# Performance work log

Hardware: AMD Instinct MI355X
Metric: run time of the kernel (lower is better)

Reference implementation:

```python
import jax, jax.numpy as jnp
import numpy as np

DT = 0.1  # Euler timestep (init kwarg)

def setup_inputs() -> dict:
    key = jax.random.key(0)
    ks = jax.random.split(key, 6)
    B, L, S, U, H = 1024, 512, 64, 32, 512
    return {
        "initial_state": jax.random.normal(ks[0], (B, S), dtype=jnp.float32),
        "control_inputs": jax.random.normal(ks[1], (B, L, U), dtype=jnp.float32),
        "W1": jax.random.normal(ks[2], (S + U, H), dtype=jnp.float32) * (1.0 / np.sqrt(S + U)),
        "b1": jnp.zeros((H,), dtype=jnp.float32),
        "W2": jax.random.normal(ks[3], (H, S), dtype=jnp.float32) * (1.0 / np.sqrt(H)),
        "b2": jnp.zeros((S,), dtype=jnp.float32),
    }

def reference(initial_state, control_inputs, W1, b1, W2, b2):
    # Euler integration: state_{t+1} = state_t + dt * f(state_t, u_t)
    # f is a 2-layer tanh MLP on the concatenated [state, control].
    def step(state, u):
        z = jnp.concatenate([state, u], axis=-1)        # (B, S+U)
        diff = jnp.tanh(z @ W1 + b1) @ W2 + b2          # (B, S)
        new_state = state + diff * DT
        return new_state, new_state

    u_seq = jnp.swapaxes(control_inputs, 0, 1)          # (L, B, U)
    _, states = jax.lax.scan(step, initial_state, u_seq)  # (L, B, S)
    return jnp.swapaxes(states, 0, 1)                   # (B, L, S)
```

## Files before the change

kernel.cpp:

```cpp
#include <hip/hip_runtime.h>
#include <hip/hip_fp16.h>


typedef _Float16 f16;
typedef __attribute__((ext_vector_type(4))) _Float16 f16x4;
typedef __attribute__((ext_vector_type(8))) _Float16 f16x8;
typedef __attribute__((ext_vector_type(4))) float f32x4;

#define MFMA16(a, b, c) __builtin_amdgcn_mfma_f32_16x16x32_f16((a), (b), (c), 0, 0, 0)

__device__ __forceinline__ float tanh_fast(float x) {
    float t = __builtin_amdgcn_exp2f(x * 2.885390081777927f);
    float r = __builtin_amdgcn_rcpf(t + 1.0f);
    return __builtin_fmaf(-2.0f, r, 1.0f);
}

__global__ __launch_bounds__(512, 2)
void euler_kernel(const float* __restrict__ init,
                  const float* __restrict__ uin,
                  const float* __restrict__ W1,
                  const float* __restrict__ b1,
                  const float* __restrict__ W2,
                  const float* __restrict__ b2,
                  float* __restrict__ out) {
    const int L = 512, S = 64, U = 32, H = 512;
    const int tid  = threadIdx.x;
    const int lane = tid & 63;
    const int w    = tid >> 6;
    const int g    = lane >> 4;
    const int r16  = lane & 15;
    const int b0   = blockIdx.x * 16;

    __shared__ f16   zbuf[6 * 64 * 8];
    __shared__ float pbuf[8 * 16 * 16 * 4];

    f16x8 W1F[6][4];
    #pragma unroll
    for (int kk = 0; kk < 6; ++kk)
      #pragma unroll
      for (int nf = 0; nf < 4; ++nf) {
          const int hcol = w * 64 + 32 * (nf >> 1) + 8 * (r16 >> 2) + 4 * (nf & 1) + (r16 & 3);
          #pragma unroll
          for (int j = 0; j < 8; ++j) {
              int k  = kk * 32 + g * 8 + j;
              int kr = (k < 128) ? (k & 63) : (64 + (k & 31));
              W1F[kk][nf][j] = (f16)W1[kr * H + hcol];
          }
      }
    f32x4 b1v[4];
    #pragma unroll
    for (int nf = 0; nf < 4; ++nf)
        b1v[nf] = *(const f32x4*)&b1[w * 64 + 32 * (nf >> 1) + 4 * (nf & 1) + 8 * g];

    f16x8 W2F[2][4];
    #pragma unroll
    for (int a = 0; a < 2; ++a)
      #pragma unroll
      for (int nf2 = 0; nf2 < 4; ++nf2)
        #pragma unroll
        for (int j = 0; j < 8; ++j) {
            int k = w * 64 + a * 32 + g * 8 + j;
            W2F[a][nf2][j] = (f16)W2[k * S + nf2 * 16 + r16];
        }

    f32x4 b2v = (f32x4){0.f, 0.f, 0.f, 0.f};
    f32x4 stateF = (f32x4){0.f, 0.f, 0.f, 0.f};
    f32x4 ua0 = (f32x4){0.f, 0.f, 0.f, 0.f}, ua1 = ua0;
    const int schunk = (w >> 1) * 64 + ((w & 1) * 2 + (g >> 1)) * 16 + r16;
    const int soff   = (g & 1) * 4;

    if (w < 4) {
        b2v    = *(const f32x4*)&b2[w * 16 + g * 4];
        stateF = *(const f32x4*)&init[(size_t)(b0 + r16) * S + w * 16 + g * 4];
        f16x4 sh, sl;
        #pragma unroll
        for (int j = 0; j < 4; ++j) {
            sh[j] = (f16)stateF[j];
            sl[j] = (f16)(stateF[j] - (float)sh[j]);
        }
        *(f16x4*)&zbuf[schunk * 8 + soff]         = sh;
        *(f16x4*)&zbuf[(schunk + 128) * 8 + soff] = sl;
    } else if (w == 4 || w == 5) {
        const float* up = uin + (size_t)(b0 + r16) * L * U + g * 8;
        f32x4 u0 = *(const f32x4*)up;
        f32x4 u1 = *(const f32x4*)(up + 4);
        f16x8 uv;
        if (w == 4) {
            #pragma unroll
            for (int j = 0; j < 4; ++j) { uv[j] = (f16)u0[j]; uv[4 + j] = (f16)u1[j]; }
            *(f16x8*)&zbuf[(256 + lane) * 8] = uv;
        } else {
            #pragma unroll
            for (int j = 0; j < 4; ++j) {
                uv[j]     = (f16)(u0[j] - (float)(f16)u0[j]);
                uv[4 + j] = (f16)(u1[j] - (float)(f16)u1[j]);
            }
            *(f16x8*)&zbuf[(320 + lane) * 8] = uv;
        }
        ua0 = *(const f32x4*)(up + U);
        ua1 = *(const f32x4*)(up + U + 4);
    }
    __syncthreads();

    #pragma unroll 1
    for (int t = 0; t < L; ++t) {
        f16x8 zf[6];
        #pragma unroll
        for (int kk = 0; kk < 6; ++kk)
            zf[kk] = *(const f16x8*)&zbuf[(kk * 64 + lane) * 8];
        f32x4 acc1[4];
        #pragma unroll
        for (int nf = 0; nf < 4; ++nf) acc1[nf] = b1v[nf];
        #pragma unroll
        for (int kk = 0; kk < 6; ++kk)
          #pragma unroll
          for (int nf = 0; nf < 4; ++nf)
            acc1[nf] = MFMA16(W1F[kk][nf], zf[kk], acc1[nf]);
        f16x8 hb[2];
        #pragma unroll
        for (int a = 0; a < 2; ++a)
          #pragma unroll
          for (int j8 = 0; j8 < 8; ++j8)
            hb[a][j8] = (f16)tanh_fast(acc1[a * 2 + (j8 >> 2)][j8 & 3]);
        f32x4 acc2[4];
        #pragma unroll
        for (int nf2 = 0; nf2 < 4; ++nf2) acc2[nf2] = (f32x4){0.f, 0.f, 0.f, 0.f};
        #pragma unroll
        for (int a = 0; a < 2; ++a)
          #pragma unroll
          for (int nf2 = 0; nf2 < 4; ++nf2)
            acc2[nf2] = MFMA16(W2F[a][nf2], hb[a], acc2[nf2]);
        #pragma unroll
        for (int nf2 = 0; nf2 < 4; ++nf2)
            *(f32x4*)&pbuf[(w * 256 + nf2 * 64 + lane) * 4] = acc2[nf2];
        __syncthreads();

        if (w < 4) {
            f32x4 sum = *(const f32x4*)&pbuf[(w * 64 + lane) * 4];
            #pragma unroll
            for (int ww = 1; ww < 8; ++ww) {
                f32x4 p = *(const f32x4*)&pbuf[(ww * 256 + w * 64 + lane) * 4];
                #pragma unroll
                for (int j = 0; j < 4; ++j) sum[j] += p[j];
            }
            f16x4 sh, sl;
            #pragma unroll
            for (int j = 0; j < 4; ++j) {
                float d = sum[j] + b2v[j];
                float s = __builtin_fmaf(0.1f, d, stateF[j]);
                stateF[j] = s;
                sh[j] = (f16)s;
                sl[j] = (f16)(s - (float)sh[j]);
            }
            *(f32x4*)&out[((size_t)(b0 + r16) * L + t) * S + w * 16 + g * 4] = stateF;
            *(f16x4*)&zbuf[schunk * 8 + soff]         = sh;
            *(f16x4*)&zbuf[(schunk + 128) * 8 + soff] = sl;
        } else if (w == 4 || w == 5) {
            if (t + 1 < L) {
                f16x8 uv;
                if (w == 4) {
                    #pragma unroll
                    for (int j = 0; j < 4; ++j) { uv[j] = (f16)ua0[j]; uv[4 + j] = (f16)ua1[j]; }
                    *(f16x8*)&zbuf[(256 + lane) * 8] = uv;
                } else {
                    #pragma unroll
                    for (int j = 0; j < 4; ++j) {
                        uv[j]     = (f16)(ua0[j] - (float)(f16)ua0[j]);
                        uv[4 + j] = (f16)(ua1[j] - (float)(f16)ua1[j]);
                    }
                    *(f16x8*)&zbuf[(320 + lane) * 8] = uv;
                }
            }
            if (t + 2 < L) {
                const float* up = uin + (size_t)(b0 + r16) * L * U + (size_t)(t + 2) * U + g * 8;
                ua0 = *(const f32x4*)up;
                ua1 = *(const f32x4*)(up + 4);
            }
        }
        __syncthreads();
    }
}

extern "C" void kernel_launch(void* const* d_in, const int* in_sizes, int n_in,
                              void* d_out, int out_size, void* d_ws, size_t ws_size,
                              hipStream_t stream) {
    const float* init = (const float*)d_in[0];
    const float* uin  = (const float*)d_in[1];
    const float* W1   = (const float*)d_in[2];
    const float* b1   = (const float*)d_in[3];
    const float* W2   = (const float*)d_in[4];
    const float* b2   = (const float*)d_in[5];
    euler_kernel<<<dim3(64), dim3(512), 0, stream>>>(init, uin, W1, b1, W2, b2,
                                                     (float*)d_out);
}
```

Before: 600.6 us.

## Precompute control-input layer-1 contribution off critical path; spread reduction across all waves

Each wave now computes the control-input part of the first-layer MFMA (hi/lo split) for the next step in registers during the current step, so the per-step dependent chain only runs four K-chunks on the state instead of six. The cross-wave reduction of layer-2 partials and the state update are spread over all eight waves (two outputs per lane) instead of four. The __syncthreads calls are replaced by a raw s_barrier preceded by an LDS-only waitcnt. This cuts serial latency per timestep but adds redundant u-MFMAs in every wave and more barrier-sensitive LDS traffic.

```diff
diff --git a/kernel.cpp b/kernel.cpp
--- a/kernel.cpp
+++ b/kernel.cpp
@@ -3,11 +3,16 @@
 
 
 typedef _Float16 f16;
-typedef __attribute__((ext_vector_type(4))) _Float16 f16x4;
+typedef __attribute__((ext_vector_type(2))) _Float16 f16x2;
 typedef __attribute__((ext_vector_type(8))) _Float16 f16x8;
+typedef __attribute__((ext_vector_type(2))) float f32x2;
 typedef __attribute__((ext_vector_type(4))) float f32x4;
 
 #define MFMA16(a, b, c) __builtin_amdgcn_mfma_f32_16x16x32_f16((a), (b), (c), 0, 0, 0)
+
+#define BAR() do { asm volatile("s_waitcnt lgkmcnt(0)" ::: "memory"); \
+                   __builtin_amdgcn_s_barrier();                      \
+                   asm volatile("" ::: "memory"); } while (0)
 
 __device__ __forceinline__ float tanh_fast(float x) {
     float t = __builtin_amdgcn_exp2f(x * 2.885390081777927f);
@@ -31,10 +36,11 @@
     const int r16  = lane & 15;
     const int b0   = blockIdx.x * 16;
 
-    __shared__ f16   zbuf[6 * 64 * 8];
-    __shared__ float pbuf[8 * 16 * 16 * 4];
+    __shared__ f16   zbuf[256 * 8];
+    __shared__ float pbuf[8 * 256 * 4];
 
-    f16x8 W1F[6][4];
+    f16x8 W1F[4][4];
+    f16x8 W1Fu[2][4];
     #pragma unroll
     for (int kk = 0; kk < 6; ++kk)
       #pragma unroll
@@ -44,7 +50,8 @@
           for (int j = 0; j < 8; ++j) {
               int k  = kk * 32 + g * 8 + j;
               int kr = (k < 128) ? (k & 63) : (64 + (k & 31));
-              W1F[kk][nf][j] = (f16)W1[kr * H + hcol];
+              f16 v  = (f16)W1[kr * H + hcol];
+              if (kk < 4) W1F[kk][nf][j] = v; else W1Fu[kk - 4][nf][j] = v;
           }
       }
     f32x4 b1v[4];
@@ -63,56 +70,53 @@
             W2F[a][nf2][j] = (f16)W2[k * S + nf2 * 16 + r16];
         }
 
-    f32x4 b2v = (f32x4){0.f, 0.f, 0.f, 0.f};
-    f32x4 stateF = (f32x4){0.f, 0.f, 0.f, 0.f};
-    f32x4 ua0 = (f32x4){0.f, 0.f, 0.f, 0.f}, ua1 = ua0;
-    const int schunk = (w >> 1) * 64 + ((w & 1) * 2 + (g >> 1)) * 16 + r16;
-    const int soff   = (g & 1) * 4;
+    f32x2 b2v    = *(const f32x2*)&b2[w * 8 + g * 2];
+    f32x2 stateF = *(const f32x2*)&init[(size_t)(b0 + r16) * S + w * 8 + g * 2];
+    const int zci = ((w >> 2) * 64 + (w & 3) * 16 + r16) * 8 + g * 2;
+    {
+        f16 h0 = (f16)stateF[0], h1 = (f16)stateF[1];
+        f16x2 hi2, lo2;
+        hi2[0] = h0;                              hi2[1] = h1;
+        lo2[0] = (f16)(stateF[0] - (float)h0);    lo2[1] = (f16)(stateF[1] - (float)h1);
+        *(f16x2*)&zbuf[zci]        = hi2;
+        *(f16x2*)&zbuf[zci + 1024] = lo2;
+    }
 
-    if (w < 4) {
-        b2v    = *(const f32x4*)&b2[w * 16 + g * 4];
-        stateF = *(const f32x4*)&init[(size_t)(b0 + r16) * S + w * 16 + g * 4];
-        f16x4 sh, sl;
+    const float* uptr = uin + (size_t)(b0 + r16) * L * U + g * 8;
+    f32x4 ua0 = *(const f32x4*)uptr;
+    f32x4 ua1 = *(const f32x4*)(uptr + 4);
+    f32x4 uacc[4];
+    #pragma unroll
+    for (int nf = 0; nf < 4; ++nf) uacc[nf] = b1v[nf];
+    {
+        f16x8 uh, ul;
         #pragma unroll
         for (int j = 0; j < 4; ++j) {
-            sh[j] = (f16)stateF[j];
-            sl[j] = (f16)(stateF[j] - (float)sh[j]);
+            f16 h0 = (f16)ua0[j]; uh[j] = h0;     ul[j] = (f16)(ua0[j] - (float)h0);
+            f16 h1 = (f16)ua1[j]; uh[4 + j] = h1; ul[4 + j] = (f16)(ua1[j] - (float)h1);
         }
-        *(f16x4*)&zbuf[schunk * 8 + soff]         = sh;
-        *(f16x4*)&zbuf[(schunk + 128) * 8 + soff] = sl;
-    } else if (w == 4 || w == 5) {
-        const float* up = uin + (size_t)(b0 + r16) * L * U + g * 8;
-        f32x4 u0 = *(const f32x4*)up;
-        f32x4 u1 = *(const f32x4*)(up + 4);
-        f16x8 uv;
-        if (w == 4) {
-            #pragma unroll
-            for (int j = 0; j < 4; ++j) { uv[j] = (f16)u0[j]; uv[4 + j] = (f16)u1[j]; }
-            *(f16x8*)&zbuf[(256 + lane) * 8] = uv;
-        } else {
-            #pragma unroll
-            for (int j = 0; j < 4; ++j) {
-                uv[j]     = (f16)(u0[j] - (float)(f16)u0[j]);
-                uv[4 + j] = (f16)(u1[j] - (float)(f16)u1[j]);
-            }
-            *(f16x8*)&zbuf[(320 + lane) * 8] = uv;
-        }
-        ua0 = *(const f32x4*)(up + U);
-        ua1 = *(const f32x4*)(up + U + 4);
+        #pragma unroll
+        for (int nf = 0; nf < 4; ++nf) uacc[nf] = MFMA16(W1Fu[0][nf], uh, uacc[nf]);
+        #pragma unroll
+        for (int nf = 0; nf < 4; ++nf) uacc[nf] = MFMA16(W1Fu[1][nf], ul, uacc[nf]);
     }
-    __syncthreads();
+    ua0 = *(const f32x4*)(uptr + U);
+    ua1 = *(const f32x4*)(uptr + U + 4);
+    BAR();
+
+    const int pbase = ((w >> 1) * 64 + (2 * (w & 1) + (g >> 1)) * 16 + r16) * 4 + 2 * (g & 1);
 
     #pragma unroll 1
     for (int t = 0; t < L; ++t) {
-        f16x8 zf[6];
+        f16x8 zf[4];
         #pragma unroll
-        for (int kk = 0; kk < 6; ++kk)
+        for (int kk = 0; kk < 4; ++kk)
             zf[kk] = *(const f16x8*)&zbuf[(kk * 64 + lane) * 8];
         f32x4 acc1[4];
         #pragma unroll
-        for (int nf = 0; nf < 4; ++nf) acc1[nf] = b1v[nf];
+        for (int nf = 0; nf < 4; ++nf) acc1[nf] = uacc[nf];
         #pragma unroll
-        for (int kk = 0; kk < 6; ++kk)
+        for (int kk = 0; kk < 4; ++kk)
           #pragma unroll
           for (int nf = 0; nf < 4; ++nf)
             acc1[nf] = MFMA16(W1F[kk][nf], zf[kk], acc1[nf]);
@@ -133,51 +137,47 @@
         #pragma unroll
         for (int nf2 = 0; nf2 < 4; ++nf2)
             *(f32x4*)&pbuf[(w * 256 + nf2 * 64 + lane) * 4] = acc2[nf2];
-        __syncthreads();
 
-        if (w < 4) {
-            f32x4 sum = *(const f32x4*)&pbuf[(w * 64 + lane) * 4];
-            #pragma unroll
-            for (int ww = 1; ww < 8; ++ww) {
-                f32x4 p = *(const f32x4*)&pbuf[(ww * 256 + w * 64 + lane) * 4];
-                #pragma unroll
-                for (int j = 0; j < 4; ++j) sum[j] += p[j];
-            }
-            f16x4 sh, sl;
+        #pragma unroll
+        for (int nf = 0; nf < 4; ++nf) uacc[nf] = b1v[nf];
+        {
+            f16x8 uh, ul;
             #pragma unroll
             for (int j = 0; j < 4; ++j) {
-                float d = sum[j] + b2v[j];
-                float s = __builtin_fmaf(0.1f, d, stateF[j]);
-                stateF[j] = s;
-                sh[j] = (f16)s;
-                sl[j] = (f16)(s - (float)sh[j]);
+                f16 h0 = (f16)ua0[j]; uh[j] = h0;     ul[j] = (f16)(ua0[j] - (float)h0);
+                f16 h1 = (f16)ua1[j]; uh[4 + j] = h1; ul[4 + j] = (f16)(ua1[j] - (float)h1);
             }
-            *(f32x4*)&out[((size_t)(b0 + r16) * L + t) * S + w * 16 + g * 4] = stateF;
-            *(f16x4*)&zbuf[schunk * 8 + soff]         = sh;
-            *(f16x4*)&zbuf[(schunk + 128) * 8 + soff] = sl;
-        } else if (w == 4 || w == 5) {
-            if (t + 1 < L) {
-                f16x8 uv;
-                if (w == 4) {
-                    #pragma unroll
-                    for (int j = 0; j < 4; ++j) { uv[j] = (f16)ua0[j]; uv[4 + j] = (f16)ua1[j]; }
-                    *(f16x8*)&zbuf[(256 + lane) * 8] = uv;
-                } else {
-                    #pragma unroll
-                    for (int j = 0; j < 4; ++j) {
-                        uv[j]     = (f16)(ua0[j] - (float)(f16)ua0[j]);
-                        uv[4 + j] = (f16)(ua1[j] - (float)(f16)ua1[j]);
-                    }
-                    *(f16x8*)&zbuf[(320 + lane) * 8] = uv;
-                }
-            }
-            if (t + 2 < L) {
-                const float* up = uin + (size_t)(b0 + r16) * L * U + (size_t)(t + 2) * U + g * 8;
-                ua0 = *(const f32x4*)up;
-                ua1 = *(const f32x4*)(up + 4);
-            }
+            #pragma unroll
+            for (int nf = 0; nf < 4; ++nf) uacc[nf] = MFMA16(W1Fu[0][nf], uh, uacc[nf]);
+            #pragma unroll
+            for (int nf = 0; nf < 4; ++nf) uacc[nf] = MFMA16(W1Fu[1][nf], ul, uacc[nf]);
         }
-        __syncthreads();
+        {
+            int tp = (t + 2 < L) ? (t + 2) : (L - 1);
+            const float* up = uptr + (size_t)tp * U;
+            ua0 = *(const f32x4*)up;
+            ua1 = *(const f32x4*)(up + 4);
+        }
+        BAR();
+
+        f32x2 sum = (f32x2){0.f, 0.f};
+        #pragma unroll
+        for (int ww = 0; ww < 8; ++ww) {
+            f32x2 p = *(const f32x2*)&pbuf[ww * 1024 + pbase];
+            sum[0] += p[0];
+            sum[1] += p[1];
+        }
+        float s0 = __builtin_fmaf(0.1f, sum[0] + b2v[0], stateF[0]);
+        float s1 = __builtin_fmaf(0.1f, sum[1] + b2v[1], stateF[1]);
+        stateF[0] = s0; stateF[1] = s1;
+        *(f32x2*)&out[((size_t)(b0 + r16) * L + t) * S + w * 8 + g * 2] = stateF;
+        f16 h0 = (f16)s0, h1 = (f16)s1;
+        f16x2 hi2, lo2;
+        hi2[0] = h0;                     hi2[1] = h1;
+        lo2[0] = (f16)(s0 - (float)h0);  lo2[1] = (f16)(s1 - (float)h1);
+        *(f16x2*)&zbuf[zci]        = hi2;
+        *(f16x2*)&zbuf[zci + 1024] = lo2;
+        BAR();
     }
 }
 
```

New measurement: 639.3 us. 1.06x slower.
